# Kernel tuning notes

Measured on AMD Instinct MI355X. Metric: run time of the kernel, lower is better.

The kernel has to match this reference:

```python
import jax, jax.numpy as jnp
import numpy as np

NUM_USERS = 100000
NUM_ITEMS = 50000
EMB = 64
N_SOC = 1000000
N_RAT = 1000000
BATCH = 16384
EPS = 1e-8


def setup_inputs() -> dict:
    key = jax.random.key(0)
    ks = jax.random.split(key, 8)
    user_emb = 0.01 * jax.random.normal(ks[0], (NUM_USERS, EMB), jnp.float32)
    item_emb = 0.01 * jax.random.normal(ks[1], (NUM_ITEMS, EMB), jnp.float32)
    users = jax.random.randint(ks[2], (BATCH,), 0, NUM_USERS)
    items = jax.random.randint(ks[3], (BATCH,), 0, NUM_ITEMS)
    social_src = jax.random.randint(ks[4], (N_SOC,), 0, NUM_USERS)
    social_dst = jax.random.randint(ks[5], (N_SOC,), 0, NUM_USERS)
    like_u = jax.random.randint(ks[6], (N_RAT,), 0, NUM_USERS)
    like_i = jax.random.randint(ks[7], (N_RAT,), 0, NUM_ITEMS)
    return {"user_emb": user_emb, "item_emb": item_emb, "users": users,
            "items": items, "social_src": social_src, "social_dst": social_dst,
            "like_u": like_u, "like_i": like_i}


def _deg(idx, num):
    # node degree as float column vector [num, 1]
    return jax.ops.segment_sum(jnp.ones((idx.shape[0],), jnp.float32), idx,
                               num_segments=num)[:, None]


def _seg_mean(msg, idx, num):
    s = jax.ops.segment_sum(msg, idx, num_segments=num)
    cnt = _deg(idx, num)
    return s / jnp.maximum(cnt, 1.0)


def reference(user_emb, item_emb, users, items, social_src, social_dst, like_u, like_i):
    # degree-based self-weights (deg=0 -> 1, deg>0 -> ~0)
    user_deg = _deg(like_u, NUM_USERS)            # out-degree on 'like'
    u_sw = 1.0 - user_deg / (user_deg + EPS)
    item_deg = _deg(like_i, NUM_ITEMS)            # out-degree on 'rev_like'
    i_sw = 1.0 - item_deg / (item_deg + EPS)

    def social_conv(hu):
        # mean aggregation over user->user social edges
        return _seg_mean(hu[social_src], social_dst, NUM_USERS)

    def rating_conv(hu, hi):
        # user <- mean of liked-item embeddings, plus degree-gated self
        new_u = u_sw * hu + _seg_mean(hi[like_i], like_u, NUM_USERS)
        new_i = i_sw * hi + _seg_mean(hu[like_u], like_i, NUM_ITEMS)
        return new_u, new_i

    # layer 1
    soc1 = social_conv(user_emb)
    rat_u1, rat_i1 = rating_conv(user_emb, item_emb)
    u1 = 0.5 * soc1 + 0.5 * rat_u1
    # layer 2 (stacked on per-branch states, as in the torch code)
    soc2 = social_conv(soc1)
    rat_u2, _ = rating_conv(rat_u1, rat_i1)
    u2 = 0.5 * soc2 + 0.5 * rat_u2

    # l_user = [0, 1, 2]
    final_user = user_emb + u1 + u2
    final_item = item_emb

    latest_user = final_user[users]
    latest_item = final_item[items]
    predict = jax.nn.sigmoid(jnp.sum(latest_user * latest_item, axis=1))
    return predict, latest_user, latest_item
```

## Files before the change

### kernel.cpp

```cpp
#include <hip/hip_runtime.h>
#include <hip/hip_bf16.h>

#define NUSERS 100000
#define NITEMS 50000
#define NEDGE  1000000
#define NBATCH 16384
#define CAP_LU 320000
#define EPB    2048
#define NBLK_E ((NEDGE + EPB - 1) / EPB)
#define NBW    3125
#define GGRID  2048

#define OFF_GC     0
#define OFF_GB     768
#define OFF_GCUR   1536
#define OFF_BITS   2304
#define OFF_NEED   (OFF_BITS + 3136)
#define OFF_ZEND   (OFF_NEED + NUSERS / 4)
#define OFF_IDEG   OFF_ZEND
#define OFF_UDEG   (OFF_IDEG + NITEMS)
#define OFF_SDEG   (OFF_UDEG + NUSERS)
#define OFF_ISTART (OFF_SDEG + NUSERS)
#define OFF_USTART (OFF_ISTART + NITEMS)
#define OFF_SSTART (OFF_USTART + NUSERS)
#define OFF_PARTLI 530464
#define OFF_PARTLU (OFF_PARTLI + NEDGE)
#define OFF_PARTSD (OFF_PARTLU + CAP_LU)
#define OFF_UEMBH  OFF_PARTLI
#define OFF_CSRLI  (OFF_UEMBH + NUSERS * 32)
#define OFF_CSRLU  (OFF_CSRLI + NEDGE)
#define OFF_CSRSD  (OFF_CSRLU + CAP_LU)
#define OFF_RI1    (OFF_CSRSD + NEDGE)
#define OFF_SOC1   (OFF_RI1 + NITEMS * 32)
#define WS_FLOATS  (OFF_SOC1 + NUSERS * 32)

typedef unsigned short u16;

__device__ __forceinline__ float bf2f(u16 h) {
    union { unsigned u; float f; } c; c.u = ((unsigned)h) << 16; return c.f;
}
__device__ __forceinline__ u16 f2bf(float f) {
    union { float f; unsigned u; } c; c.f = f;
    unsigned r = c.u + 0x7fffu + ((c.u >> 16) & 1u);
    return (u16)(r >> 16);
}
__device__ __forceinline__ void acc2(unsigned w, float& a0, float& a1) {
    a0 += bf2f((u16)(w & 0xffff));
    a1 += bf2f((u16)(w >> 16));
}
__device__ __forceinline__ void acc8(uint4 w, float* a) {
    acc2(w.x, a[0], a[1]); acc2(w.y, a[2], a[3]);
    acc2(w.z, a[4], a[5]); acc2(w.w, a[6], a[7]);
}

__global__ void k_slot(const int* __restrict__ users, unsigned* __restrict__ bits,
                       unsigned char* __restrict__ needed) {
    int b = blockIdx.x * blockDim.x + threadIdx.x;
    if (b < NBATCH) {
        int u = users[b];
        atomicOr(&bits[u >> 5], 1u << (u & 31));
        needed[u] = 1;
    }
}

__global__ void k_passA(const int* __restrict__ lu, const int* __restrict__ li,
                        const int* __restrict__ sd, const int* __restrict__ ss,
                        const unsigned* __restrict__ bits, int* __restrict__ gcnt,
                        unsigned char* __restrict__ needed) {
    __shared__ int lc[768];
    __shared__ unsigned sbits[NBW];
    int t = threadIdx.x;
    for (int k = t; k < 768; k += 256) lc[k] = 0;
    for (int k = t; k < NBW; k += 256) sbits[k] = bits[k];
    __syncthreads();
    int base = blockIdx.x * EPB;
    int end = base + EPB; if (end > NEDGE) end = NEDGE;
    for (int e = base + t; e < end; e += 256) {
        int item = li[e], a = lu[e], d = sd[e];
        atomicAdd(&lc[item >> 9], 1);
        if ((sbits[a >> 5] >> (a & 31)) & 1)
            atomicAdd(&lc[256 + (a >> 9)], 1);
        atomicAdd(&lc[512 + (d >> 9)], 1);
        if ((sbits[d >> 5] >> (d & 31)) & 1)
            needed[ss[e]] = 1;
    }
    __syncthreads();
    for (int k = t; k < 768; k += 256)
        if (lc[k]) atomicAdd(&gcnt[k], lc[k]);
}

__global__ void k_passB(const int* __restrict__ gcnt, int* __restrict__ gbase,
                        int* __restrict__ gcur) {
    __shared__ int s[256];
    int t = threadIdx.x;
    for (int j = 0; j < 3; ++j) {
        int v = gcnt[j * 256 + t];
        s[t] = v;
        __syncthreads();
        for (int o = 1; o < 256; o <<= 1) {
            int x = (t >= o) ? s[t - o] : 0;
            __syncthreads();
            s[t] += x;
            __syncthreads();
        }
        int ex = s[t] - v;
        gbase[j * 256 + t] = ex;
        gcur[j * 256 + t] = ex;
        __syncthreads();
    }
}

__global__ void k_passC(const int* __restrict__ lu, const int* __restrict__ li,
                        const int* __restrict__ sd, const int* __restrict__ ss,
                        const unsigned* __restrict__ bits, int* __restrict__ gcur,
                        int* __restrict__ partLI, int* __restrict__ partLU,
                        int* __restrict__ partSD) {
    __shared__ int lc[768];
    __shared__ int go[768];
    __shared__ unsigned sbits[NBW];
    int t = threadIdx.x;
    for (int k = t; k < 768; k += 256) lc[k] = 0;
    for (int k = t; k < NBW; k += 256) sbits[k] = bits[k];
    __syncthreads();
    int base = blockIdx.x * EPB;
    int end = base + EPB; if (end > NEDGE) end = NEDGE;
    unsigned mask = 0;
    int i = 0;
    for (int e = base + t; e < end; e += 256, ++i) {
        int item = li[e], a = lu[e], d = sd[e];
        atomicAdd(&lc[item >> 9], 1);
        if ((sbits[a >> 5] >> (a & 31)) & 1) {
            atomicAdd(&lc[256 + (a >> 9)], 1);
            mask |= (1u << i);
        }
        atomicAdd(&lc[512 + (d >> 9)], 1);
    }
    __syncthreads();
    for (int k = t; k < 768; k += 256) {
        go[k] = lc[k] ? atomicAdd(&gcur[k], lc[k]) : 0;
        lc[k] = 0;
    }
    __syncthreads();
    i = 0;
    for (int e = base + t; e < end; e += 256, ++i) {
        int item = li[e], a = lu[e], d = sd[e], s_ = ss[e];
        int b0 = item >> 9;
        int r0 = atomicAdd(&lc[b0], 1);
        partLI[go[b0] + r0] = (a << 9) | (item & 511);
        if (mask & (1u << i)) {
            int b1 = 256 + (a >> 9);
            int r1 = atomicAdd(&lc[b1], 1);
            partLU[go[b1] + r1] = (item << 9) | (a & 511);
        }
        int b2 = 512 + (d >> 9);
        int r2 = atomicAdd(&lc[b2], 1);
        partSD[go[b2] + r2] = (s_ << 9) | (d & 511);
    }
}

__global__ void k_passD(const int* __restrict__ gcnt, const int* __restrict__ gbase,
                        const int* __restrict__ partLI, const int* __restrict__ partLU,
                        const int* __restrict__ partSD, int* __restrict__ csrli,
                        int* __restrict__ csrlu, int* __restrict__ csrsd,
                        int* __restrict__ ideg, int* __restrict__ udeg,
                        int* __restrict__ sdeg, int* __restrict__ istart,
                        int* __restrict__ ustart, int* __restrict__ sstart) {
    __shared__ int lcnt[512], lstart[512], sb[2][512];
    int t = threadIdx.x;
    int blk = blockIdx.x, list, b;
    const int* part; int* csr; int* deg; int* start; int n;
    if (blk < 196)      { list = 0; b = blk;       part = partLI; csr = csrli; deg = ideg; start = istart; n = NITEMS; }
    else if (blk < 392) { list = 1; b = blk - 196; part = partLU; csr = csrlu; deg = udeg; start = ustart; n = NUSERS; }
    else                { list = 2; b = blk - 392; part = partSD; csr = csrsd; deg = sdeg; start = sstart; n = NUSERS; }
    int base = gbase[list * 256 + b], cnt = gcnt[list * 256 + b];
    int node0 = b << 9;
    int M = n - node0; if (M > 512) M = 512; if (M < 0) M = 0;

    lcnt[t] = 0; lcnt[t + 256] = 0;
    __syncthreads();
    for (int i = t; i < cnt; i += 256) atomicAdd(&lcnt[part[base + i] & 511], 1);
    __syncthreads();
    sb[0][t] = lcnt[t]; sb[0][t + 256] = lcnt[t + 256];
    __syncthreads();
    int pp = 0;
    for (int o = 1; o < 512; o <<= 1) {
        int np = pp ^ 1;
        for (int k = t; k < 512; k += 256) {
            int v = sb[pp][k];
            if (k >= o) v += sb[pp][k - o];
            sb[np][k] = v;
        }
        __syncthreads();
        pp = np;
    }
    for (int k = t; k < 512; k += 256) {
        int ex = sb[pp][k] - lcnt[k];
        lstart[k] = ex;
        if (k < M) { deg[node0 + k] = lcnt[k]; start[node0 + k] = base + ex; }
    }
    __syncthreads();
    lcnt[t] = 0; lcnt[t + 256] = 0;
    __syncthreads();
    for (int i = t; i < cnt; i += 256) {
        int p = part[base + i];
        int nl = p & 511;
        int r = atomicAdd(&lcnt[nl], 1);
        csr[base + lstart[nl] + r] = p >> 9;
    }
}

__global__ void k_cvt(const float* __restrict__ src, u16* __restrict__ dst) {
    int t = blockIdx.x * 256 + threadIdx.x;
    if (t >= NUSERS * 16) return;
    float4 v = ((const float4*)src)[t];
    ushort4 o;
    o.x = f2bf(v.x); o.y = f2bf(v.y); o.z = f2bf(v.z); o.w = f2bf(v.w);
    ((ushort4*)dst)[t] = o;
}

__device__ __forceinline__ void item_store(int n, int dg, const float* __restrict__ iemb,
                                           unsigned* __restrict__ ri1, int l8,
                                           const float* __restrict__ s) {
    float dgf = (float)dg;
    float inv = 1.0f / fmaxf(dgf, 1.0f);
    float sw  = 1.0f - dgf / (dgf + 1e-8f);
    float4 e0 = ((const float4*)(iemb + n * 64))[l8 * 2];
    float4 e1 = ((const float4*)(iemb + n * 64))[l8 * 2 + 1];
    uint4 o;
    o.x = (unsigned)f2bf(sw * e0.x + s[0] * inv) | ((unsigned)f2bf(sw * e0.y + s[1] * inv) << 16);
    o.y = (unsigned)f2bf(sw * e0.z + s[2] * inv) | ((unsigned)f2bf(sw * e0.w + s[3] * inv) << 16);
    o.z = (unsigned)f2bf(sw * e1.x + s[4] * inv) | ((unsigned)f2bf(sw * e1.y + s[5] * inv) << 16);
    o.w = (unsigned)f2bf(sw * e1.z + s[6] * inv) | ((unsigned)f2bf(sw * e1.w + s[7] * inv) << 16);
    ((uint4*)(ri1 + n * 32))[l8] = o;
}
__device__ __forceinline__ void soc_store(int n, int dg, unsigned* __restrict__ soc1, int l8,
                                          const float* __restrict__ s) {
    float inv = 1.0f / fmaxf((float)dg, 1.0f);
    uint4 o;
    o.x = (unsigned)f2bf(s[0] * inv) | ((unsigned)f2bf(s[1] * inv) << 16);
    o.y = (unsigned)f2bf(s[2] * inv) | ((unsigned)f2bf(s[3] * inv) << 16);
    o.z = (unsigned)f2bf(s[4] * inv) | ((unsigned)f2bf(s[5] * inv) << 16);
    o.w = (unsigned)f2bf(s[6] * inv) | ((unsigned)f2bf(s[7] * inv) << 16);
    ((uint4*)(soc1 + n * 32))[l8] = o;
}

__device__ __forceinline__ void gather_pair(const unsigned* __restrict__ uh32,
                                            const int* __restrict__ csr,
                                            int jA, int dA, int jB, int dB,
                                            int lane, int g, int l8,
                                            float* __restrict__ aA,
                                            float* __restrict__ aB) {
    int cA = (lane < dA) ? csr[jA + lane] : 0;
    int cB = (lane < dB) ? csr[jB + lane] : 0;
    int kmA = dA < 64 ? dA : 64;
    int kmB = dB < 64 ? dB : 64;
    int clA = kmA > 0 ? kmA - 1 : 0;
    int clB = kmB > 0 ? kmB - 1 : 0;
    int km  = kmA > kmB ? kmA : kmB;
    for (int k = 0; k < km; k += 16) {
        int q0 = k + g, q1 = k + 8 + g;
        int iA0 = q0 < kmA ? q0 : clA;
        int iA1 = q1 < kmA ? q1 : clA;
        int iB0 = q0 < kmB ? q0 : clB;
        int iB1 = q1 < kmB ? q1 : clB;
        int rA0 = __shfl(cA, iA0), rA1 = __shfl(cA, iA1);
        int rB0 = __shfl(cB, iB0), rB1 = __shfl(cB, iB1);
        uint4 wA0 = *(const uint4*)(uh32 + rA0 * 32 + l8 * 4);
        uint4 wA1 = *(const uint4*)(uh32 + rA1 * 32 + l8 * 4);
        uint4 wB0 = *(const uint4*)(uh32 + rB0 * 32 + l8 * 4);
        uint4 wB1 = *(const uint4*)(uh32 + rB1 * 32 + l8 * 4);
        if (q0 < kmA) acc8(wA0, aA);
        if (q1 < kmA) acc8(wA1, aA);
        if (q0 < kmB) acc8(wB0, aB);
        if (q1 < kmB) acc8(wB1, aB);
    }
    for (int k = 64; k < dA; k += 8) {
        int q = k + g; int idx = q < dA ? q : dA - 1;
        int r = csr[jA + idx];
        uint4 w = *(const uint4*)(uh32 + r * 32 + l8 * 4);
        if (q < dA) acc8(w, aA);
    }
    for (int k = 64; k < dB; k += 8) {
        int q = k + g; int idx = q < dB ? q : dB - 1;
        int r = csr[jB + idx];
        uint4 w = *(const uint4*)(uh32 + r * 32 + l8 * 4);
        if (q < dB) acc8(w, aB);
    }
    #pragma unroll
    for (int off = 8; off <= 32; off <<= 1) {
        #pragma unroll
        for (int m = 0; m < 8; ++m) {
            aA[m] += __shfl_xor(aA[m], off);
            aB[m] += __shfl_xor(aB[m], off);
        }
    }
}

__global__ void k_gather_fused(const float* __restrict__ iemb,
                               const unsigned* __restrict__ uh32,
                               const int* __restrict__ csrli, const int* __restrict__ istart,
                               const int* __restrict__ ideg, unsigned* __restrict__ ri1,
                               const int* __restrict__ csrsd, const int* __restrict__ sstart,
                               const int* __restrict__ sdeg,
                               const unsigned char* __restrict__ needed,
                               unsigned* __restrict__ soc1) {
    int lane = threadIdx.x & 63;
    int wid  = blockIdx.x * 4 + (threadIdx.x >> 6);
    int nw   = gridDim.x * 4;
    int g = lane >> 3, l8 = lane & 7;
    const int NPI = NITEMS / 2;
    const int NP  = NPI + NUSERS / 2;
    for (int w = wid; w < NP; w += nw) {
        if (w < NPI) {
            int nA = w * 2, nB = nA + 1;
            int jA = istart[nA], dA = ideg[nA];
            int jB = istart[nB], dB = ideg[nB];
            float aA[8] = {0.f,0.f,0.f,0.f,0.f,0.f,0.f,0.f};
            float aB[8] = {0.f,0.f,0.f,0.f,0.f,0.f,0.f,0.f};
            gather_pair(uh32, csrli, jA, dA, jB, dB, lane, g, l8, aA, aB);
            if (g == 0)      item_store(nA, dA, iemb, ri1, l8, aA);
            else if (g == 1) item_store(nB, dB, iemb, ri1, l8, aB);
        } else {
            int nA = (w - NPI) * 2, nB = nA + 1;
            unsigned short nd = *(const unsigned short*)(needed + nA);
            if (!nd) continue;
            int needA = nd & 0xff, needB = nd >> 8;
            int jA = sstart[nA], dA = needA ? sdeg[nA] : 0;
            int jB = sstart[nB], dB = needB ? sdeg[nB] : 0;
            float aA[8] = {0.f,0.f,0.f,0.f,0.f,0.f,0.f,0.f};
            float aB[8] = {0.f,0.f,0.f,0.f,0.f,0.f,0.f,0.f};
            gather_pair(uh32, csrsd, jA, dA, jB, dB, lane, g, l8, aA, aB);
            if (g == 0 && needA)      soc_store(nA, dA, soc1, l8, aA);
            else if (g == 1 && needB) soc_store(nB, dB, soc1, l8, aB);
        }
    }
}

__global__ void k_final2(const int* __restrict__ users, const int* __restrict__ items,
                         const float* __restrict__ uemb, const float* __restrict__ iemb,
                         const u16* __restrict__ ri1, const int* __restrict__ csrlu,
                         const int* __restrict__ ustart, const int* __restrict__ udeg,
                         const u16* __restrict__ soc1, const int* __restrict__ csrsd,
                         const int* __restrict__ sstart, const int* __restrict__ sdeg,
                         float* __restrict__ out) {
    int d   = threadIdx.x & 63;
    int wid = blockIdx.x * 4 + (threadIdx.x >> 6);
    int nw  = gridDim.x * 4;
    for (int b = wid; b < NBATCH; b += nw) {
        int u = users[b], it = items[b];
        int ju = ustart[u], du = udeg[u];
        int js = sstart[u], ds = sdeg[u];
        int cvU = (d < du) ? csrlu[ju + d] : 0;
        int cvS = (d < ds) ? csrsd[js + d] : 0;
        int kmu = du < 64 ? du : 64;
        int clu = kmu > 0 ? kmu - 1 : 0;
        float p0=0.f,p1=0.f,p2=0.f,p3=0.f, q0=0.f,q1=0.f,q2=0.f,q3=0.f;
        for (int k = 0; k < kmu; k += 8) {
            int x1 = k+1 < kmu ? k+1 : clu, x2 = k+2 < kmu ? k+2 : clu;
            int x3 = k+3 < kmu ? k+3 : clu, x4 = k+4 < kmu ? k+4 : clu;
            int x5 = k+5 < kmu ? k+5 : clu, x6 = k+6 < kmu ? k+6 : clu;
            int x7 = k+7 < kmu ? k+7 : clu;
            int i0 = __shfl(cvU, k),  i1 = __shfl(cvU, x1);
            int i2 = __shfl(cvU, x2), i3 = __shfl(cvU, x3);
            int i4 = __shfl(cvU, x4), i5 = __shfl(cvU, x5);
            int i6 = __shfl(cvU, x6), i7 = __shfl(cvU, x7);
            float t0 = iemb[i0 * 64 + d], t1 = iemb[i1 * 64 + d];
            float t2 = iemb[i2 * 64 + d], t3 = iemb[i3 * 64 + d];
            float t4 = iemb[i4 * 64 + d], t5 = iemb[i5 * 64 + d];
            float t6 = iemb[i6 * 64 + d], t7 = iemb[i7 * 64 + d];
            float r0 = bf2f(ri1[i0 * 64 + d]), r1 = bf2f(ri1[i1 * 64 + d]);
            float r2 = bf2f(ri1[i2 * 64 + d]), r3 = bf2f(ri1[i3 * 64 + d]);
            float r4 = bf2f(ri1[i4 * 64 + d]), r5 = bf2f(ri1[i5 * 64 + d]);
            float r6 = bf2f(ri1[i6 * 64 + d]), r7 = bf2f(ri1[i7 * 64 + d]);
            p0 += t0; q0 += r0;
            if (k+1 < kmu) { p1 += t1; q1 += r1; }
            if (k+2 < kmu) { p2 += t2; q2 += r2; }
            if (k+3 < kmu) { p3 += t3; q3 += r3; }
            if (k+4 < kmu) { p0 += t4; q0 += r4; }
            if (k+5 < kmu) { p1 += t5; q1 += r5; }
            if (k+6 < kmu) { p2 += t6; q2 += r6; }
            if (k+7 < kmu) { p3 += t7; q3 += r7; }
        }
        for (int j = ju + 64; j < ju + du; ++j) {
            int i0 = csrlu[j];
            p0 += iemb[i0 * 64 + d]; q0 += bf2f(ri1[i0 * 64 + d]);
        }
        int kms = ds < 64 ? ds : 64;
        int cls = kms > 0 ? kms - 1 : 0;
        float s0=0.f, s1a=0.f, s2a=0.f, s3a=0.f;
        for (int k = 0; k < kms; k += 8) {
            int x1 = k+1 < kms ? k+1 : cls, x2 = k+2 < kms ? k+2 : cls;
            int x3 = k+3 < kms ? k+3 : cls, x4 = k+4 < kms ? k+4 : cls;
            int x5 = k+5 < kms ? k+5 : cls, x6 = k+6 < kms ? k+6 : cls;
            int x7 = k+7 < kms ? k+7 : cls;
            int c0 = __shfl(cvS, k),  c1 = __shfl(cvS, x1);
            int c2 = __shfl(cvS, x2), c3 = __shfl(cvS, x3);
            int c4 = __shfl(cvS, x4), c5 = __shfl(cvS, x5);
            int c6 = __shfl(cvS, x6), c7 = __shfl(cvS, x7);
            float f0 = bf2f(soc1[c0 * 64 + d]), f1 = bf2f(soc1[c1 * 64 + d]);
            float f2 = bf2f(soc1[c2 * 64 + d]), f3 = bf2f(soc1[c3 * 64 + d]);
            float f4 = bf2f(soc1[c4 * 64 + d]), f5 = bf2f(soc1[c5 * 64 + d]);
            float f6 = bf2f(soc1[c6 * 64 + d]), f7 = bf2f(soc1[c7 * 64 + d]);
            s0 += f0;
            if (k+1 < kms) s1a += f1;
            if (k+2 < kms) s2a += f2;
            if (k+3 < kms) s3a += f3;
            if (k+4 < kms) s0  += f4;
            if (k+5 < kms) s1a += f5;
            if (k+6 < kms) s2a += f6;
            if (k+7 < kms) s3a += f7;
        }
        for (int j = js + 64; j < js + ds; ++j)
            s0 += bf2f(soc1[csrsd[j] * 64 + d]);
        float invU = 1.0f / fmaxf((float)du, 1.0f);
        float ru1 = ((p0 + p1) + (p2 + p3)) * invU;
        float ru2 = ((q0 + q1) + (q2 + q3)) * invU;
        float s2 = ((s0 + s1a) + (s2a + s3a)) / fmaxf((float)ds, 1.0f);
        float ud = (float)du;
        float usw = 1.0f - ud / (ud + 1e-8f);
        float ue = uemb[u * 64 + d];
        float s1 = bf2f(soc1[u * 64 + d]);
        float r1 = usw * ue + ru1;
        float r2 = usw * r1 + ru2;
        float fu = ue + 0.5f * (s1 + r1) + 0.5f * (s2 + r2);
        float iv = iemb[it * 64 + d];
        out[NBATCH + b * 64 + d]               = fu;
        out[NBATCH + NBATCH * 64 + b * 64 + d] = iv;
        float p = fu * iv;
        #pragma unroll
        for (int o = 32; o > 0; o >>= 1) p += __shfl_down(p, o);
        if (d == 0) out[b] = 1.0f / (1.0f + __expf(-p));
    }
}

extern "C" void kernel_launch(void* const* d_in, const int* in_sizes, int n_in,
                              void* d_out, int out_size, void* d_ws, size_t ws_size,
                              hipStream_t stream) {
    const float* uemb  = (const float*)d_in[0];
    const float* iemb  = (const float*)d_in[1];
    const int*   users = (const int*)d_in[2];
    const int*   items = (const int*)d_in[3];
    const int*   ssrc  = (const int*)d_in[4];
    const int*   sdst  = (const int*)d_in[5];
    const int*   lu    = (const int*)d_in[6];
    const int*   li    = (const int*)d_in[7];
    float* out = (float*)d_out;

    if (ws_size < (size_t)WS_FLOATS * 4) return;

    int*           W      = (int*)d_ws;
    int*           gcnt   = W + OFF_GC;
    int*           gbase  = W + OFF_GB;
    int*           gcur   = W + OFF_GCUR;
    unsigned*      bits   = (unsigned*)(W + OFF_BITS);
    unsigned char* needed = (unsigned char*)(W + OFF_NEED);
    int*           ideg   = W + OFF_IDEG;
    int*           udeg   = W + OFF_UDEG;
    int*           sdeg   = W + OFF_SDEG;
    int*           istart = W + OFF_ISTART;
    int*           ustart = W + OFF_USTART;
    int*           sstart = W + OFF_SSTART;
    int*           partLI = W + OFF_PARTLI;
    int*           partLU = W + OFF_PARTLU;
    int*           partSD = W + OFF_PARTSD;
    u16*           uembh  = (u16*)(W + OFF_UEMBH);
    int*           csrli  = W + OFF_CSRLI;
    int*           csrlu  = W + OFF_CSRLU;
    int*           csrsd  = W + OFF_CSRSD;
    u16*           ri1    = (u16*)(W + OFF_RI1);
    u16*           soc1   = (u16*)(W + OFF_SOC1);

    hipMemsetAsync(d_ws, 0, (size_t)OFF_ZEND * 4, stream);

    const int B = 256;

    k_slot<<<(NBATCH + B - 1) / B, B, 0, stream>>>(users, bits, needed);
    k_passA<<<NBLK_E, B, 0, stream>>>(lu, li, sdst, ssrc, bits, gcnt, needed);
    k_passB<<<1, B, 0, stream>>>(gcnt, gbase, gcur);
    k_passC<<<NBLK_E, B, 0, stream>>>(lu, li, sdst, ssrc, bits, gcur,
                                      partLI, partLU, partSD);
    k_passD<<<588, B, 0, stream>>>(gcnt, gbase, partLI, partLU, partSD,
                                   csrli, csrlu, csrsd, ideg, udeg, sdeg,
                                   istart, ustart, sstart);

    k_cvt<<<(NUSERS * 16 + B - 1) / B, B, 0, stream>>>(uemb, uembh);

    k_gather_fused<<<GGRID, B, 0, stream>>>(iemb, (const unsigned*)uembh,
                                            csrli, istart, ideg, (unsigned*)ri1,
                                            csrsd, sstart, sdeg, needed,
                                            (unsigned*)soc1);

    k_final2<<<GGRID, B, 0, stream>>>(users, items, uemb, iemb, ri1, csrlu,
                                      ustart, udeg, soc1, csrsd, sstart, sdeg, out);
}
```

Measured before the change: 252.6 us.

## Interleave bf16 item embeddings with rating state and pair batch rows per wave

Builds an interleaved bf16 record per item that holds the converted raw item embedding next to the layer-1 rating state, so the final gather reads one 256-byte record per neighbor instead of a float row plus a separate bf16 row. The fp32-to-bf16 conversion of user and item embeddings is merged with the batch-slot marking into a single init kernel, and the separate conversion launch is removed. The final kernel now processes two batch rows per wave with 4-way unrolling to expose more independent loads. In exchange, the raw item mean is now accumulated from bf16 values, which lowers precision. The workspace is also relaid out so the converted buffers no longer alias the partition arrays.

```diff
diff --git a/kernel.cpp b/kernel.cpp
--- a/kernel.cpp
+++ b/kernel.cpp
@@ -10,6 +10,8 @@
 #define NBLK_E ((NEDGE + EPB - 1) / EPB)
 #define NBW    3125
 #define GGRID  2048
+#define NB_CVT 9375
+#define NB_INIT (NB_CVT + (NBATCH + 255) / 256)
 
 #define OFF_GC     0
 #define OFF_GB     768
@@ -23,16 +25,16 @@
 #define OFF_ISTART (OFF_SDEG + NUSERS)
 #define OFF_USTART (OFF_ISTART + NITEMS)
 #define OFF_SSTART (OFF_USTART + NUSERS)
-#define OFF_PARTLI 530464
+#define OFF_UEMBH  530464
+#define OFF_REC    (OFF_UEMBH + NUSERS * 32)
+#define OFF_SOC1   (OFF_REC + NITEMS * 64)
+#define OFF_PARTLI (OFF_SOC1 + NUSERS * 32)
 #define OFF_PARTLU (OFF_PARTLI + NEDGE)
 #define OFF_PARTSD (OFF_PARTLU + CAP_LU)
-#define OFF_UEMBH  OFF_PARTLI
-#define OFF_CSRLI  (OFF_UEMBH + NUSERS * 32)
+#define OFF_CSRLI  (OFF_PARTSD + NEDGE)
 #define OFF_CSRLU  (OFF_CSRLI + NEDGE)
 #define OFF_CSRSD  (OFF_CSRLU + CAP_LU)
-#define OFF_RI1    (OFF_CSRSD + NEDGE)
-#define OFF_SOC1   (OFF_RI1 + NITEMS * 32)
-#define WS_FLOATS  (OFF_SOC1 + NUSERS * 32)
+#define WS_FLOATS  (OFF_CSRSD + NEDGE)
 
 typedef unsigned short u16;
 
@@ -53,13 +55,33 @@
     acc2(w.z, a[4], a[5]); acc2(w.w, a[6], a[7]);
 }
 
-__global__ void k_slot(const int* __restrict__ users, unsigned* __restrict__ bits,
+__global__ void k_init(const float* __restrict__ uemb, const float* __restrict__ iemb,
+                       const int* __restrict__ users, u16* __restrict__ uembh,
+                       u16* __restrict__ rec, unsigned* __restrict__ bits,
                        unsigned char* __restrict__ needed) {
-    int b = blockIdx.x * blockDim.x + threadIdx.x;
-    if (b < NBATCH) {
-        int u = users[b];
-        atomicOr(&bits[u >> 5], 1u << (u & 31));
-        needed[u] = 1;
+    int blk = blockIdx.x;
+    if (blk < NB_CVT) {
+        int t = blk * 256 + threadIdx.x;
+        if (t < NUSERS * 16) {
+            float4 v = ((const float4*)uemb)[t];
+            ushort4 o;
+            o.x = f2bf(v.x); o.y = f2bf(v.y); o.z = f2bf(v.z); o.w = f2bf(v.w);
+            ((ushort4*)uembh)[t] = o;
+        } else {
+            int t2 = t - NUSERS * 16;
+            int i = t2 >> 4, c = t2 & 15;
+            float4 v = ((const float4*)iemb)[t2];
+            ushort4 o;
+            o.x = f2bf(v.x); o.y = f2bf(v.y); o.z = f2bf(v.z); o.w = f2bf(v.w);
+            ((ushort4*)rec)[i * 32 + c] = o;
+        }
+    } else {
+        int b = (blk - NB_CVT) * 256 + threadIdx.x;
+        if (b < NBATCH) {
+            int u = users[b];
+            atomicOr(&bits[u >> 5], 1u << (u & 31));
+            needed[u] = 1;
+        }
     }
 }
 
@@ -209,17 +231,8 @@
     }
 }
 
-__global__ void k_cvt(const float* __restrict__ src, u16* __restrict__ dst) {
-    int t = blockIdx.x * 256 + threadIdx.x;
-    if (t >= NUSERS * 16) return;
-    float4 v = ((const float4*)src)[t];
-    ushort4 o;
-    o.x = f2bf(v.x); o.y = f2bf(v.y); o.z = f2bf(v.z); o.w = f2bf(v.w);
-    ((ushort4*)dst)[t] = o;
-}
-
 __device__ __forceinline__ void item_store(int n, int dg, const float* __restrict__ iemb,
-                                           unsigned* __restrict__ ri1, int l8,
+                                           u16* __restrict__ rec, int l8,
                                            const float* __restrict__ s) {
     float dgf = (float)dg;
     float inv = 1.0f / fmaxf(dgf, 1.0f);
@@ -231,7 +244,7 @@
     o.y = (unsigned)f2bf(sw * e0.z + s[2] * inv) | ((unsigned)f2bf(sw * e0.w + s[3] * inv) << 16);
     o.z = (unsigned)f2bf(sw * e1.x + s[4] * inv) | ((unsigned)f2bf(sw * e1.y + s[5] * inv) << 16);
     o.w = (unsigned)f2bf(sw * e1.z + s[6] * inv) | ((unsigned)f2bf(sw * e1.w + s[7] * inv) << 16);
-    ((uint4*)(ri1 + n * 32))[l8] = o;
+    ((uint4*)(rec + n * 128 + 64))[l8] = o;
 }
 __device__ __forceinline__ void soc_store(int n, int dg, unsigned* __restrict__ soc1, int l8,
                                           const float* __restrict__ s) {
@@ -299,7 +312,7 @@
 __global__ void k_gather_fused(const float* __restrict__ iemb,
                                const unsigned* __restrict__ uh32,
                                const int* __restrict__ csrli, const int* __restrict__ istart,
-                               const int* __restrict__ ideg, unsigned* __restrict__ ri1,
+                               const int* __restrict__ ideg, u16* __restrict__ rec,
                                const int* __restrict__ csrsd, const int* __restrict__ sstart,
                                const int* __restrict__ sdeg,
                                const unsigned char* __restrict__ needed,
@@ -318,8 +331,8 @@
             float aA[8] = {0.f,0.f,0.f,0.f,0.f,0.f,0.f,0.f};
             float aB[8] = {0.f,0.f,0.f,0.f,0.f,0.f,0.f,0.f};
             gather_pair(uh32, csrli, jA, dA, jB, dB, lane, g, l8, aA, aB);
-            if (g == 0)      item_store(nA, dA, iemb, ri1, l8, aA);
-            else if (g == 1) item_store(nB, dB, iemb, ri1, l8, aB);
+            if (g == 0)      item_store(nA, dA, iemb, rec, l8, aA);
+            else if (g == 1) item_store(nB, dB, iemb, rec, l8, aB);
         } else {
             int nA = (w - NPI) * 2, nB = nA + 1;
             unsigned short nd = *(const unsigned short*)(needed + nA);
@@ -338,98 +351,133 @@
 
 __global__ void k_final2(const int* __restrict__ users, const int* __restrict__ items,
                          const float* __restrict__ uemb, const float* __restrict__ iemb,
-                         const u16* __restrict__ ri1, const int* __restrict__ csrlu,
+                         const u16* __restrict__ rec, const int* __restrict__ csrlu,
                          const int* __restrict__ ustart, const int* __restrict__ udeg,
                          const u16* __restrict__ soc1, const int* __restrict__ csrsd,
                          const int* __restrict__ sstart, const int* __restrict__ sdeg,
                          float* __restrict__ out) {
     int d   = threadIdx.x & 63;
     int wid = blockIdx.x * 4 + (threadIdx.x >> 6);
-    int nw  = gridDim.x * 4;
-    for (int b = wid; b < NBATCH; b += nw) {
-        int u = users[b], it = items[b];
-        int ju = ustart[u], du = udeg[u];
-        int js = sstart[u], ds = sdeg[u];
-        int cvU = (d < du) ? csrlu[ju + d] : 0;
-        int cvS = (d < ds) ? csrsd[js + d] : 0;
-        int kmu = du < 64 ? du : 64;
-        int clu = kmu > 0 ? kmu - 1 : 0;
-        float p0=0.f,p1=0.f,p2=0.f,p3=0.f, q0=0.f,q1=0.f,q2=0.f,q3=0.f;
-        for (int k = 0; k < kmu; k += 8) {
-            int x1 = k+1 < kmu ? k+1 : clu, x2 = k+2 < kmu ? k+2 : clu;
-            int x3 = k+3 < kmu ? k+3 : clu, x4 = k+4 < kmu ? k+4 : clu;
-            int x5 = k+5 < kmu ? k+5 : clu, x6 = k+6 < kmu ? k+6 : clu;
-            int x7 = k+7 < kmu ? k+7 : clu;
-            int i0 = __shfl(cvU, k),  i1 = __shfl(cvU, x1);
-            int i2 = __shfl(cvU, x2), i3 = __shfl(cvU, x3);
-            int i4 = __shfl(cvU, x4), i5 = __shfl(cvU, x5);
-            int i6 = __shfl(cvU, x6), i7 = __shfl(cvU, x7);
-            float t0 = iemb[i0 * 64 + d], t1 = iemb[i1 * 64 + d];
-            float t2 = iemb[i2 * 64 + d], t3 = iemb[i3 * 64 + d];
-            float t4 = iemb[i4 * 64 + d], t5 = iemb[i5 * 64 + d];
-            float t6 = iemb[i6 * 64 + d], t7 = iemb[i7 * 64 + d];
-            float r0 = bf2f(ri1[i0 * 64 + d]), r1 = bf2f(ri1[i1 * 64 + d]);
-            float r2 = bf2f(ri1[i2 * 64 + d]), r3 = bf2f(ri1[i3 * 64 + d]);
-            float r4 = bf2f(ri1[i4 * 64 + d]), r5 = bf2f(ri1[i5 * 64 + d]);
-            float r6 = bf2f(ri1[i6 * 64 + d]), r7 = bf2f(ri1[i7 * 64 + d]);
-            p0 += t0; q0 += r0;
-            if (k+1 < kmu) { p1 += t1; q1 += r1; }
-            if (k+2 < kmu) { p2 += t2; q2 += r2; }
-            if (k+3 < kmu) { p3 += t3; q3 += r3; }
-            if (k+4 < kmu) { p0 += t4; q0 += r4; }
-            if (k+5 < kmu) { p1 += t5; q1 += r5; }
-            if (k+6 < kmu) { p2 += t6; q2 += r6; }
-            if (k+7 < kmu) { p3 += t7; q3 += r7; }
-        }
-        for (int j = ju + 64; j < ju + du; ++j) {
-            int i0 = csrlu[j];
-            p0 += iemb[i0 * 64 + d]; q0 += bf2f(ri1[i0 * 64 + d]);
-        }
-        int kms = ds < 64 ? ds : 64;
-        int cls = kms > 0 ? kms - 1 : 0;
-        float s0=0.f, s1a=0.f, s2a=0.f, s3a=0.f;
-        for (int k = 0; k < kms; k += 8) {
-            int x1 = k+1 < kms ? k+1 : cls, x2 = k+2 < kms ? k+2 : cls;
-            int x3 = k+3 < kms ? k+3 : cls, x4 = k+4 < kms ? k+4 : cls;
-            int x5 = k+5 < kms ? k+5 : cls, x6 = k+6 < kms ? k+6 : cls;
-            int x7 = k+7 < kms ? k+7 : cls;
-            int c0 = __shfl(cvS, k),  c1 = __shfl(cvS, x1);
-            int c2 = __shfl(cvS, x2), c3 = __shfl(cvS, x3);
-            int c4 = __shfl(cvS, x4), c5 = __shfl(cvS, x5);
-            int c6 = __shfl(cvS, x6), c7 = __shfl(cvS, x7);
-            float f0 = bf2f(soc1[c0 * 64 + d]), f1 = bf2f(soc1[c1 * 64 + d]);
-            float f2 = bf2f(soc1[c2 * 64 + d]), f3 = bf2f(soc1[c3 * 64 + d]);
-            float f4 = bf2f(soc1[c4 * 64 + d]), f5 = bf2f(soc1[c5 * 64 + d]);
-            float f6 = bf2f(soc1[c6 * 64 + d]), f7 = bf2f(soc1[c7 * 64 + d]);
-            s0 += f0;
-            if (k+1 < kms) s1a += f1;
-            if (k+2 < kms) s2a += f2;
-            if (k+3 < kms) s3a += f3;
-            if (k+4 < kms) s0  += f4;
-            if (k+5 < kms) s1a += f5;
-            if (k+6 < kms) s2a += f6;
-            if (k+7 < kms) s3a += f7;
-        }
-        for (int j = js + 64; j < js + ds; ++j)
-            s0 += bf2f(soc1[csrsd[j] * 64 + d]);
-        float invU = 1.0f / fmaxf((float)du, 1.0f);
-        float ru1 = ((p0 + p1) + (p2 + p3)) * invU;
-        float ru2 = ((q0 + q1) + (q2 + q3)) * invU;
-        float s2 = ((s0 + s1a) + (s2a + s3a)) / fmaxf((float)ds, 1.0f);
-        float ud = (float)du;
+    if (wid >= NBATCH / 2) return;
+    int bA = wid, bB = wid + NBATCH / 2;
+    int uA = users[bA], uB = users[bB];
+    int itA = items[bA], itB = items[bB];
+    int juA = ustart[uA], duA = udeg[uA];
+    int juB = ustart[uB], duB = udeg[uB];
+    int jsA = sstart[uA], dsA = sdeg[uA];
+    int jsB = sstart[uB], dsB = sdeg[uB];
+    int cvUA = (d < duA) ? csrlu[juA + d] : 0;
+    int cvUB = (d < duB) ? csrlu[juB + d] : 0;
+    int cvSA = (d < dsA) ? csrsd[jsA + d] : 0;
+    int cvSB = (d < dsB) ? csrsd[jsB + d] : 0;
+    int kmuA = duA < 64 ? duA : 64, cluA = kmuA > 0 ? kmuA - 1 : 0;
+    int kmuB = duB < 64 ? duB : 64, cluB = kmuB > 0 ? kmuB - 1 : 0;
+    int kmu = kmuA > kmuB ? kmuA : kmuB;
+    float pA0=0.f,pA1=0.f,pA2=0.f,pA3=0.f, qA0=0.f,qA1=0.f,qA2=0.f,qA3=0.f;
+    float pB0=0.f,pB1=0.f,pB2=0.f,pB3=0.f, qB0=0.f,qB1=0.f,qB2=0.f,qB3=0.f;
+    for (int k = 0; k < kmu; k += 4) {
+        int xA0 = k   < kmuA ? k   : cluA, xA1 = k+1 < kmuA ? k+1 : cluA;
+        int xA2 = k+2 < kmuA ? k+2 : cluA, xA3 = k+3 < kmuA ? k+3 : cluA;
+        int xB0 = k   < kmuB ? k   : cluB, xB1 = k+1 < kmuB ? k+1 : cluB;
+        int xB2 = k+2 < kmuB ? k+2 : cluB, xB3 = k+3 < kmuB ? k+3 : cluB;
+        int iA0 = __shfl(cvUA, xA0), iA1 = __shfl(cvUA, xA1);
+        int iA2 = __shfl(cvUA, xA2), iA3 = __shfl(cvUA, xA3);
+        int iB0 = __shfl(cvUB, xB0), iB1 = __shfl(cvUB, xB1);
+        int iB2 = __shfl(cvUB, xB2), iB3 = __shfl(cvUB, xB3);
+        float tA0 = bf2f(rec[iA0*128 + d]),    tA1 = bf2f(rec[iA1*128 + d]);
+        float tA2 = bf2f(rec[iA2*128 + d]),    tA3 = bf2f(rec[iA3*128 + d]);
+        float rA0 = bf2f(rec[iA0*128 + 64 + d]), rA1 = bf2f(rec[iA1*128 + 64 + d]);
+        float rA2 = bf2f(rec[iA2*128 + 64 + d]), rA3 = bf2f(rec[iA3*128 + 64 + d]);
+        float tB0 = bf2f(rec[iB0*128 + d]),    tB1 = bf2f(rec[iB1*128 + d]);
+        float tB2 = bf2f(rec[iB2*128 + d]),    tB3 = bf2f(rec[iB3*128 + d]);
+        float rB0 = bf2f(rec[iB0*128 + 64 + d]), rB1 = bf2f(rec[iB1*128 + 64 + d]);
+        float rB2 = bf2f(rec[iB2*128 + 64 + d]), rB3 = bf2f(rec[iB3*128 + 64 + d]);
+        if (k   < kmuA) { pA0 += tA0; qA0 += rA0; }
+        if (k+1 < kmuA) { pA1 += tA1; qA1 += rA1; }
+        if (k+2 < kmuA) { pA2 += tA2; qA2 += rA2; }
+        if (k+3 < kmuA) { pA3 += tA3; qA3 += rA3; }
+        if (k   < kmuB) { pB0 += tB0; qB0 += rB0; }
+        if (k+1 < kmuB) { pB1 += tB1; qB1 += rB1; }
+        if (k+2 < kmuB) { pB2 += tB2; qB2 += rB2; }
+        if (k+3 < kmuB) { pB3 += tB3; qB3 += rB3; }
+    }
+    for (int j = juA + 64; j < juA + duA; ++j) {
+        int i0 = csrlu[j];
+        pA0 += bf2f(rec[i0*128 + d]); qA0 += bf2f(rec[i0*128 + 64 + d]);
+    }
+    for (int j = juB + 64; j < juB + duB; ++j) {
+        int i0 = csrlu[j];
+        pB0 += bf2f(rec[i0*128 + d]); qB0 += bf2f(rec[i0*128 + 64 + d]);
+    }
+    int kmsA = dsA < 64 ? dsA : 64, clsA = kmsA > 0 ? kmsA - 1 : 0;
+    int kmsB = dsB < 64 ? dsB : 64, clsB = kmsB > 0 ? kmsB - 1 : 0;
+    int kms = kmsA > kmsB ? kmsA : kmsB;
+    float sA0=0.f,sA1=0.f,sA2=0.f,sA3=0.f, sB0=0.f,sB1=0.f,sB2=0.f,sB3=0.f;
+    for (int k = 0; k < kms; k += 4) {
+        int xA0 = k   < kmsA ? k   : clsA, xA1 = k+1 < kmsA ? k+1 : clsA;
+        int xA2 = k+2 < kmsA ? k+2 : clsA, xA3 = k+3 < kmsA ? k+3 : clsA;
+        int xB0 = k   < kmsB ? k   : clsB, xB1 = k+1 < kmsB ? k+1 : clsB;
+        int xB2 = k+2 < kmsB ? k+2 : clsB, xB3 = k+3 < kmsB ? k+3 : clsB;
+        int cA0 = __shfl(cvSA, xA0), cA1 = __shfl(cvSA, xA1);
+        int cA2 = __shfl(cvSA, xA2), cA3 = __shfl(cvSA, xA3);
+        int cB0 = __shfl(cvSB, xB0), cB1 = __shfl(cvSB, xB1);
+        int cB2 = __shfl(cvSB, xB2), cB3 = __shfl(cvSB, xB3);
+        float fA0 = bf2f(soc1[cA0*64 + d]), fA1 = bf2f(soc1[cA1*64 + d]);
+        float fA2 = bf2f(soc1[cA2*64 + d]), fA3 = bf2f(soc1[cA3*64 + d]);
+        float fB0 = bf2f(soc1[cB0*64 + d]), fB1 = bf2f(soc1[cB1*64 + d]);
+        float fB2 = bf2f(soc1[cB2*64 + d]), fB3 = bf2f(soc1[cB3*64 + d]);
+        if (k   < kmsA) sA0 += fA0;
+        if (k+1 < kmsA) sA1 += fA1;
+        if (k+2 < kmsA) sA2 += fA2;
+        if (k+3 < kmsA) sA3 += fA3;
+        if (k   < kmsB) sB0 += fB0;
+        if (k+1 < kmsB) sB1 += fB1;
+        if (k+2 < kmsB) sB2 += fB2;
+        if (k+3 < kmsB) sB3 += fB3;
+    }
+    for (int j = jsA + 64; j < jsA + dsA; ++j)
+        sA0 += bf2f(soc1[csrsd[j]*64 + d]);
+    for (int j = jsB + 64; j < jsB + dsB; ++j)
+        sB0 += bf2f(soc1[csrsd[j]*64 + d]);
+    {
+        float invU = 1.0f / fmaxf((float)duA, 1.0f);
+        float ru1 = ((pA0 + pA1) + (pA2 + pA3)) * invU;
+        float ru2 = ((qA0 + qA1) + (qA2 + qA3)) * invU;
+        float s2 = ((sA0 + sA1) + (sA2 + sA3)) / fmaxf((float)dsA, 1.0f);
+        float ud = (float)duA;
         float usw = 1.0f - ud / (ud + 1e-8f);
-        float ue = uemb[u * 64 + d];
-        float s1 = bf2f(soc1[u * 64 + d]);
+        float ue = uemb[uA * 64 + d];
+        float s1 = bf2f(soc1[uA * 64 + d]);
         float r1 = usw * ue + ru1;
         float r2 = usw * r1 + ru2;
         float fu = ue + 0.5f * (s1 + r1) + 0.5f * (s2 + r2);
-        float iv = iemb[it * 64 + d];
-        out[NBATCH + b * 64 + d]               = fu;
-        out[NBATCH + NBATCH * 64 + b * 64 + d] = iv;
+        float iv = iemb[itA * 64 + d];
+        out[NBATCH + bA * 64 + d]               = fu;
+        out[NBATCH + NBATCH * 64 + bA * 64 + d] = iv;
         float p = fu * iv;
         #pragma unroll
         for (int o = 32; o > 0; o >>= 1) p += __shfl_down(p, o);
-        if (d == 0) out[b] = 1.0f / (1.0f + __expf(-p));
+        if (d == 0) out[bA] = 1.0f / (1.0f + __expf(-p));
+    }
+    {
+        float invU = 1.0f / fmaxf((float)duB, 1.0f);
+        float ru1 = ((pB0 + pB1) + (pB2 + pB3)) * invU;
+        float ru2 = ((qB0 + qB1) + (qB2 + qB3)) * invU;
+        float s2 = ((sB0 + sB1) + (sB2 + sB3)) / fmaxf((float)dsB, 1.0f);
+        float ud = (float)duB;
+        float usw = 1.0f - ud / (ud + 1e-8f);
+        float ue = uemb[uB * 64 + d];
+        float s1 = bf2f(soc1[uB * 64 + d]);
+        float r1 = usw * ue + ru1;
+        float r2 = usw * r1 + ru2;
+        float fu = ue + 0.5f * (s1 + r1) + 0.5f * (s2 + r2);
+        float iv = iemb[itB * 64 + d];
+        out[NBATCH + bB * 64 + d]               = fu;
+        out[NBATCH + NBATCH * 64 + bB * 64 + d] = iv;
+        float p = fu * iv;
+        #pragma unroll
+        for (int o = 32; o > 0; o >>= 1) p += __shfl_down(p, o);
+        if (d == 0) out[bB] = 1.0f / (1.0f + __expf(-p));
     }
 }
 
@@ -460,21 +508,22 @@
     int*           istart = W + OFF_ISTART;
     int*           ustart = W + OFF_USTART;
     int*           sstart = W + OFF_SSTART;
+    u16*           uembh  = (u16*)(W + OFF_UEMBH);
+    u16*           rec    = (u16*)(W + OFF_REC);
+    u16*           soc1   = (u16*)(W + OFF_SOC1);
     int*           partLI = W + OFF_PARTLI;
     int*           partLU = W + OFF_PARTLU;
     int*           partSD = W + OFF_PARTSD;
-    u16*           uembh  = (u16*)(W + OFF_UEMBH);
     int*           csrli  = W + OFF_CSRLI;
     int*           csrlu  = W + OFF_CSRLU;
     int*           csrsd  = W + OFF_CSRSD;
-    u16*           ri1    = (u16*)(W + OFF_RI1);
-    u16*           soc1   = (u16*)(W + OFF_SOC1);
 
     hipMemsetAsync(d_ws, 0, (size_t)OFF_ZEND * 4, stream);
 
     const int B = 256;
 
-    k_slot<<<(NBATCH + B - 1) / B, B, 0, stream>>>(users, bits, needed);
+    k_init<<<NB_INIT, B, 0, stream>>>(uemb, iemb, users, uembh, rec, bits, needed);
+
     k_passA<<<NBLK_E, B, 0, stream>>>(lu, li, sdst, ssrc, bits, gcnt, needed);
     k_passB<<<1, B, 0, stream>>>(gcnt, gbase, gcur);
     k_passC<<<NBLK_E, B, 0, stream>>>(lu, li, sdst, ssrc, bits, gcur,
@@ -483,13 +532,11 @@
                                    csrli, csrlu, csrsd, ideg, udeg, sdeg,
                                    istart, ustart, sstart);
 
-    k_cvt<<<(NUSERS * 16 + B - 1) / B, B, 0, stream>>>(uemb, uembh);
-
     k_gather_fused<<<GGRID, B, 0, stream>>>(iemb, (const unsigned*)uembh,
-                                            csrli, istart, ideg, (unsigned*)ri1,
+                                            csrli, istart, ideg, rec,
                                             csrsd, sstart, sdeg, needed,
                                             (unsigned*)soc1);
 
-    k_final2<<<GGRID, B, 0, stream>>>(users, items, uemb, iemb, ri1, csrlu,
-                                      ustart, udeg, soc1, csrsd, sstart, sdeg, out);
-}
+    k_final2<<<2048, B, 0, stream>>>(users, items, uemb, iemb, rec, csrlu,
+                                     ustart, udeg, soc1, csrsd, sstart, sdeg, out);
+}
```

Result: no change. 254.2 us (+0.6%).
